# Performance work log

Hardware: AMD Instinct MI355X
Metric: run time of the kernel (lower is better)

## Reference

```python
import jax, jax.numpy as jnp
import numpy as np

S, B, E, H = 2048, 4, 512, 8
HD = E // H


def setup_inputs() -> dict:
    key = jax.random.key(0)
    ks = jax.random.split(key, 5)
    scale = 1.0 / np.sqrt(E)
    return {
        "query": jax.random.normal(ks[0], (S, B, E), jnp.float32),
        "key": jax.random.normal(ks[1], (S, B, E), jnp.float32),
        "value": jax.random.normal(ks[2], (S, B, E), jnp.float32),
        "in_proj_weight": jax.random.normal(ks[3], (3 * E, E), jnp.float32) * scale,
        "in_proj_bias": jnp.zeros((3 * E,), jnp.float32),
        "out_proj_weight": jax.random.normal(ks[4], (E, E), jnp.float32) * scale,
        "out_proj_bias": jnp.zeros((E,), jnp.float32),
    }


def reference(query, key, value, in_proj_weight, in_proj_bias, out_proj_weight, out_proj_bias):
    tgt_len, bsz, embed_dim = query.shape
    src_len = key.shape[0]
    # Quirk of this module: first chunk (w_qk) projects BOTH q and k; third chunk projects v.
    w_qk = in_proj_weight[:embed_dim]
    w_v = in_proj_weight[2 * embed_dim:]
    b_qk = in_proj_bias[:embed_dim]
    b_v = in_proj_bias[2 * embed_dim:]
    q = query @ w_qk.T + b_qk          # [S, B, E]
    k = key @ w_qk.T + b_qk
    v = value @ w_v.T + b_v
    # (S, B, E) -> (B*H, S, HD)
    def split_heads(x, n):
        return x.reshape(n, bsz * H, HD).transpose(1, 0, 2)
    q = split_heads(q, tgt_len) / jnp.sqrt(jnp.asarray(HD, q.dtype))
    k = split_heads(k, src_len)
    v = split_heads(v, src_len)
    scores = jnp.einsum("bqd,bkd->bqk", q, k)          # [B*H, S, S] full score matrix
    attn = jax.nn.softmax(scores, axis=-1)
    out = jnp.einsum("bqk,bkd->bqd", attn, v)          # [B*H, S, HD]
    out = out.transpose(1, 0, 2).reshape(tgt_len * bsz, embed_dim)
    out = out @ out_proj_weight.T + out_proj_bias
    return out.reshape(tgt_len, bsz, embed_dim)
```

## Files before the change

### kernel.cpp

```cpp
#include <hip/hip_runtime.h>
#include <hip/hip_bf16.h>

typedef __attribute__((ext_vector_type(8))) short s16x8;
typedef __attribute__((ext_vector_type(4))) short s16x4;
typedef __attribute__((ext_vector_type(4))) float f32x4;

#if __has_builtin(__builtin_amdgcn_exp2f)
#define EXP2F(x) __builtin_amdgcn_exp2f(x)
#else
#define EXP2F(x) exp2f(x)
#endif

#define S_LEN 2048
#define EMB   512
#define MROWS 8192

__device__ __forceinline__ short f2bf(float f) {
    union { float f; unsigned u; } z; z.f = f;
    unsigned r = z.u + 0x7FFF + ((z.u >> 16) & 1);
    return (short)(r >> 16);
}
__device__ __forceinline__ short f2bf_fast(float f) {
    union { float f; unsigned u; } z; z.f = f;
    return (short)((z.u + 0x8000u) >> 16);
}
__device__ __forceinline__ int swzs(int s) { return s ^ ((s >> 3) & 7); }

template<int AF32, int BF32>
__device__ __forceinline__ void gemm_mainloop(const void* __restrict__ Ag,
                                              const void* __restrict__ Bg,
                                              short* sA, short* sB,
                                              f32x4 acc[2][4], int K)
{
    const int tid  = threadIdx.x;
    const int lane = tid & 63;
    const int wv   = tid >> 6;
    const int lsw  = lane ^ ((lane >> 3) & 7);
    const int amt  = (wv >> 1) * 2;
    const int bnt  = (wv & 1) * 4;

    const int brow = tid >> 2, bqd = tid & 3;
    const int boff = swzs((brow >> 4) * 64 + bqd * 16 + (brow & 15)) * 8;
    const int frow = tid >> 3, ffc = tid & 7;
    const int foff = swzs((frow >> 4) * 64 + (ffc >> 1) * 16 + (frow & 15)) * 8
                   + (ffc & 1) * 4;

    f32x4 afr[2], bfr[2];
    s16x8 ahr, bhr;

    auto loadT = [&](const void* G, int kt, f32x4* fr, s16x8& hr, int F32) {
        if (F32) {
            const float* g = (const float*)G + (size_t)frow * K + kt + ffc * 4;
            fr[0] = *(const f32x4*)g;
            fr[1] = *(const f32x4*)(g + (size_t)64 * K);
        } else {
            hr = *(const s16x8*)((const short*)G + (size_t)brow * K + kt + bqd * 8);
        }
    };
    auto commitT = [&](short* s, f32x4* fr, s16x8& hr, int F32) {
        if (F32) {
#pragma unroll
            for (int p = 0; p < 2; ++p) {
                s16x4 o4;
                o4[0] = f2bf_fast(fr[p][0]); o4[1] = f2bf_fast(fr[p][1]);
                o4[2] = f2bf_fast(fr[p][2]); o4[3] = f2bf_fast(fr[p][3]);
                *(s16x4*)(s + foff + p * 2048) = o4;
            }
        } else {
            *(s16x8*)(s + boff) = hr;
        }
    };

    loadT(Ag, 0, afr, ahr, AF32);
    loadT(Bg, 0, bfr, bhr, BF32);
    commitT(sA, afr, ahr, AF32);
    commitT(sB, bfr, bhr, BF32);
    __syncthreads();

    int cur = 0;
    for (int kt = 0; kt < K; kt += 32) {
        const int ktn = (kt + 32 < K) ? kt + 32 : 0;
        loadT(Ag, ktn, afr, ahr, AF32);
        loadT(Bg, ktn, bfr, bhr, BF32);

        const short* sAc = sA + cur * 4096;
        const short* sBc = sB + cur * 4096;
        s16x8 aF[2], bF[4];
#pragma unroll
        for (int i = 0; i < 2; ++i)
            aF[i] = *(const s16x8*)(sAc + ((amt + i) * 64 + lsw) * 8);
#pragma unroll
        for (int j = 0; j < 4; ++j)
            bF[j] = *(const s16x8*)(sBc + ((bnt + j) * 64 + lsw) * 8);
#pragma unroll
        for (int i = 0; i < 2; ++i)
#pragma unroll
            for (int j = 0; j < 4; ++j)
                acc[i][j] = __builtin_amdgcn_mfma_f32_16x16x32_bf16(aF[i], bF[j], acc[i][j], 0, 0, 0);

        commitT(sA + (cur ^ 1) * 4096, afr, ahr, AF32);
        commitT(sB + (cur ^ 1) * 4096, bfr, bhr, BF32);
        __syncthreads();
        cur ^= 1;
    }
}

__global__ __launch_bounds__(512, 4) void qkv_proj(const float* __restrict__ query,
                                                   const float* __restrict__ key,
                                                   const float* __restrict__ value,
                                                   const float* __restrict__ W,
                                                   const float* __restrict__ bias,
                                                   short* __restrict__ q,
                                                   short* __restrict__ k,
                                                   short* __restrict__ vt)
{
    __shared__ __align__(16) short smem[16384];
    short* sA = smem;
    short* sB = smem + 8192;

    const int z = blockIdx.z;
    const float* X  = (z == 0) ? query : (z == 1) ? key : value;
    const float* Wz = W    + (z == 2 ? (size_t)1024 * EMB : 0);
    const float* bz = bias + (z == 2 ? 1024 : 0);
    const float scale = (z == 0) ? 0.125f * 1.44269504f : 1.0f;

    const int blockM = blockIdx.x * 128, blockN = blockIdx.y * 128;

    f32x4 acc[2][4];
#pragma unroll
    for (int i = 0; i < 2; ++i)
#pragma unroll
        for (int j = 0; j < 4; ++j)
            acc[i][j] = (f32x4){0.f, 0.f, 0.f, 0.f};

    gemm_mainloop<1, 1>(X + (size_t)blockM * EMB, Wz + (size_t)blockN * EMB,
                        sA, sB, acc, EMB);

    const int tid = threadIdx.x, lane = tid & 63, wv = tid >> 6;
    const int l15 = lane & 15, quad = lane >> 4;
    const int wm = (wv >> 1) * 32, wn = (wv & 1) * 64;

#pragma unroll
    for (int j = 0; j < 4; ++j) {
        int colL = wn + j * 16 + l15;
        float bval = bz[blockN + colL];
        int hL = colL >> 6, hd = colL & 63;
#pragma unroll
        for (int i = 0; i < 2; ++i) {
#pragma unroll
            for (int r = 0; r < 4; ++r) {
                int rowL = wm + i * 16 + quad * 4 + r;
                int b = rowL & 3, sp = rowL >> 2;
                float val = (acc[i][j][r] + bval) * scale;
                int idx;
                if (z == 2) {
                    int R = (b * 2 + hL) * 64 + hd;
                    idx = R * 32 + (((sp >> 3) ^ (R & 3)) << 3) + (sp & 7);
                } else {
                    idx = ((b * 2 + hL) * 32 + sp) * 64 + hd;
                }
                smem[idx] = f2bf(val);
            }
        }
    }
    __syncthreads();

    if (z == 2) {
        int R = tid;
        int b = tid >> 7, hL = (tid >> 6) & 1, hd = tid & 63;
        int h = (blockN >> 6) + hL;
        short* dst = vt + ((size_t)(b * 8 + h) * 64 + hd) * 2048 + (blockM >> 2);
#pragma unroll
        for (int u = 0; u < 4; ++u)
            ((s16x8*)dst)[u] = *(const s16x8*)(smem + R * 32 + ((u ^ (R & 3)) << 3));
    } else {
        const s16x8* src = (const s16x8*)(smem + tid * 32);
        int b = tid >> 7, hL = (tid >> 6) & 1;
        int sp = (tid >> 1) & 31, hdh = (tid & 1) * 32;
        int h = (blockN >> 6) + hL;
        short* dstp = (z == 0) ? q : k;
        short* dst = dstp + ((size_t)(b * 8 + h) * 2048 + (blockM >> 2) + sp) * 64 + hdh;
#pragma unroll
        for (int u = 0; u < 4; ++u) ((s16x8*)dst)[u] = src[u];
    }
}

__global__ __launch_bounds__(256, 2) void flash_attn(const short* __restrict__ q,
                                                     const short* __restrict__ k,
                                                     const short* __restrict__ vt,
                                                     short* __restrict__ attn)
{
    __shared__ __align__(16) short sK[2][4096];
    __shared__ __align__(16) short sV[2][4096];
    const int bh = blockIdx.x;
    const int q0 = blockIdx.y * 128;
    const int tid = threadIdx.x, wv = tid >> 6, lane = tid & 63;
    const int l15 = lane & 15, quad = lane >> 4;
    const int lsw = lane ^ ((lane >> 3) & 7);

    s16x8 qf[2][2];
#pragma unroll
    for (int qr = 0; qr < 2; ++qr) {
        const short* qp = q + ((size_t)(bh * 2048 + q0 + wv * 32 + qr * 16 + l15)) * 64 + quad * 8;
        qf[qr][0] = *(const s16x8*)qp;
        qf[qr][1] = *(const s16x8*)(qp + 32);
    }

    const short* kg = k  + (size_t)bh * 2048 * 64;
    const short* vg = vt + (size_t)bh * 64 * 2048;

    const int rk = tid >> 2, qd = tid & 3;
    const int pr = (rk & 35) | ((rk & 24) >> 1) | ((rk & 4) << 2);
    const int kw0 = swzs((pr >> 4) * 64 + qd * 16 + (pr & 15)) * 8;
    const int vw0 = swzs((rk >> 4) * 64 + qd * 16 + (rk & 15)) * 8;
    const short* kgt = kg + (size_t)rk * 64 + qd * 8;
    const short* vgt = vg + (size_t)rk * 2048 + qd * 8;

    f32x4 o[2][4];
    float ls[2][4];
#pragma unroll
    for (int qr = 0; qr < 2; ++qr)
#pragma unroll
        for (int i = 0; i < 4; ++i) { o[qr][i] = (f32x4){0.f, 0.f, 0.f, 0.f}; ls[qr][i] = 0.f; }

    s16x8 ka = *(const s16x8*)(kgt);
    s16x8 kb = *(const s16x8*)(kgt + 32);
    s16x8 va = *(const s16x8*)(vgt);
    s16x8 vb = *(const s16x8*)(vgt + 32);
    *(s16x8*)(sK[0] + kw0)        = ka;
    *(s16x8*)(sK[0] + kw0 + 2048) = kb;
    *(s16x8*)(sV[0] + vw0)        = va;
    *(s16x8*)(sV[0] + vw0 + 2048) = vb;
    __syncthreads();

    int cur = 0;
    for (int kt = 0; kt < 2048; kt += 64) {
        const int ktn = (kt + 64) & 2047;
        ka = *(const s16x8*)(kgt + (size_t)ktn * 64);
        kb = *(const s16x8*)(kgt + (size_t)ktn * 64 + 32);
        va = *(const s16x8*)(vgt + ktn);
        vb = *(const s16x8*)(vgt + ktn + 32);

        const short* Kc = sK[cur];
        const short* Vc = sV[cur];

        f32x4 sc[2][4];
#pragma unroll
        for (int ct = 0; ct < 4; ++ct) {
            s16x8 kf0 = *(const s16x8*)(Kc + (ct * 64 + lsw) * 8);
            s16x8 kf1 = *(const s16x8*)(Kc + (ct * 64 + lsw) * 8 + 2048);
#pragma unroll
            for (int qr = 0; qr < 2; ++qr) {
                f32x4 c = (f32x4){0.f, 0.f, 0.f, 0.f};
                c = __builtin_amdgcn_mfma_f32_16x16x32_bf16(kf0, qf[qr][0], c, 0, 0, 0);
                c = __builtin_amdgcn_mfma_f32_16x16x32_bf16(kf1, qf[qr][1], c, 0, 0, 0);
                sc[qr][ct] = c;
            }
        }
        s16x8 pf[2][2];
#pragma unroll
        for (int qr = 0; qr < 2; ++qr)
#pragma unroll
            for (int c = 0; c < 2; ++c)
#pragma unroll
                for (int h = 0; h < 2; ++h)
#pragma unroll
                    for (int r = 0; r < 4; ++r) {
                        float p = EXP2F(sc[qr][2 * c + h][r]);
                        ls[qr][r] += p;
                        pf[qr][c][h * 4 + r] = f2bf_fast(p);
                    }
#pragma unroll
        for (int nt = 0; nt < 4; ++nt)
#pragma unroll
            for (int c = 0; c < 2; ++c) {
                s16x8 vf = *(const s16x8*)(Vc + ((c * 4 + nt) * 64 + lsw) * 8);
#pragma unroll
                for (int qr = 0; qr < 2; ++qr)
                    o[qr][nt] = __builtin_amdgcn_mfma_f32_16x16x32_bf16(pf[qr][c], vf, o[qr][nt], 0, 0, 0);
            }
        *(s16x8*)(sK[cur ^ 1] + kw0)        = ka;
        *(s16x8*)(sK[cur ^ 1] + kw0 + 2048) = kb;
        *(s16x8*)(sV[cur ^ 1] + vw0)        = va;
        *(s16x8*)(sV[cur ^ 1] + vw0 + 2048) = vb;
        __syncthreads();
        cur ^= 1;
    }

    const int b = bh >> 3, h = bh & 7;
#pragma unroll
    for (int qr = 0; qr < 2; ++qr) {
        float s = ls[qr][0] + ls[qr][1] + ls[qr][2] + ls[qr][3];
        s += __shfl_xor(s, 16, 64);
        s += __shfl_xor(s, 32, 64);
        float sinv = 1.0f / s;
        float inv[4];
#pragma unroll
        for (int r = 0; r < 4; ++r)
            inv[r] = __shfl(sinv, quad * 20 + r, 64);
#pragma unroll
        for (int r = 0; r < 4; ++r) {
            int srow = q0 + wv * 32 + qr * 16 + quad * 4 + r;
#pragma unroll
            for (int nt = 0; nt < 4; ++nt)
                attn[(size_t)(srow * 4 + b) * 512 + h * 64 + nt * 16 + l15] = f2bf(o[qr][nt][r] * inv[r]);
        }
    }
}

__global__ __launch_bounds__(512, 4) void out_proj(const short* __restrict__ attn,
                                                   const float* __restrict__ W,
                                                   const float* __restrict__ bias,
                                                   float* __restrict__ out)
{
    __shared__ __align__(16) short sA[2 * 4096], sB[2 * 4096];
    const int blockM = blockIdx.x * 128, blockN = blockIdx.y * 128;

    f32x4 acc[2][4];
#pragma unroll
    for (int i = 0; i < 2; ++i)
#pragma unroll
        for (int j = 0; j < 4; ++j)
            acc[i][j] = (f32x4){0.f, 0.f, 0.f, 0.f};

    gemm_mainloop<0, 1>(attn + (size_t)blockM * EMB, W + (size_t)blockN * EMB,
                        sA, sB, acc, EMB);

    const int tid = threadIdx.x, lane = tid & 63, wv = tid >> 6;
    const int l15 = lane & 15, quad = lane >> 4;
    const int wm = (wv >> 1) * 32, wn = (wv & 1) * 64;

#pragma unroll
    for (int j = 0; j < 4; ++j) {
        int col = blockN + wn + j * 16 + l15;
        float bval = bias[col];
#pragma unroll
        for (int i = 0; i < 2; ++i) {
#pragma unroll
            for (int r = 0; r < 4; ++r) {
                int row = blockM + wm + i * 16 + quad * 4 + r;
                out[(size_t)row * 512 + col] = acc[i][j][r] + bval;
            }
        }
    }
}

extern "C" void kernel_launch(void* const* d_in, const int* in_sizes, int n_in,
                              void* d_out, int out_size, void* d_ws, size_t ws_size,
                              hipStream_t stream)
{
    const float* query = (const float*)d_in[0];
    const float* key   = (const float*)d_in[1];
    const float* value = (const float*)d_in[2];
    const float* ipw   = (const float*)d_in[3];
    const float* ipb   = (const float*)d_in[4];
    const float* opw   = (const float*)d_in[5];
    const float* opb   = (const float*)d_in[6];
    float* out = (float*)d_out;

    const size_t NELEM = (size_t)MROWS * EMB;
    short* q    = (short*)d_ws;
    short* k    = q + NELEM;
    short* attn = k + NELEM;
    short* vt   = (short*)d_out;

    qkv_proj  <<<dim3(64, 4, 3), 512, 0, stream>>>(query, key, value, ipw, ipb, q, k, vt);
    flash_attn<<<dim3(32, 16),   256, 0, stream>>>(q, k, vt, attn);
    out_proj  <<<dim3(64, 4),    512, 0, stream>>>(attn, opw, opb, out);
}
```

Baseline: 202.9 us.

## Pre-convert projection weights to bf16 and deepen GEMM prefetch to two stages

```diff
diff --git a/kernel.cpp b/kernel.cpp
--- a/kernel.cpp
+++ b/kernel.cpp
@@ -25,6 +25,20 @@
     return (short)((z.u + 0x8000u) >> 16);
 }
 __device__ __forceinline__ int swzs(int s) { return s ^ ((s >> 3) & 7); }
+
+__global__ __launch_bounds__(256) void w_to_bf16(const float* __restrict__ W,
+                                                 short* __restrict__ wb, int n)
+{
+    int i = (blockIdx.x * 256 + threadIdx.x) * 8;
+    if (i < n) {
+        f32x4 a = *(const f32x4*)(W + i);
+        f32x4 b = *(const f32x4*)(W + i + 4);
+        s16x8 o;
+        o[0] = f2bf(a[0]); o[1] = f2bf(a[1]); o[2] = f2bf(a[2]); o[3] = f2bf(a[3]);
+        o[4] = f2bf(b[0]); o[5] = f2bf(b[1]); o[6] = f2bf(b[2]); o[7] = f2bf(b[3]);
+        *(s16x8*)(wb + i) = o;
+    }
+}
 
 template<int AF32, int BF32>
 __device__ __forceinline__ void gemm_mainloop(const void* __restrict__ Ag,
@@ -45,19 +59,28 @@
     const int foff = swzs((frow >> 4) * 64 + (ffc >> 1) * 16 + (frow & 15)) * 8
                    + (ffc & 1) * 4;
 
-    f32x4 afr[2], bfr[2];
-    s16x8 ahr, bhr;
-
-    auto loadT = [&](const void* G, int kt, f32x4* fr, s16x8& hr, int F32) {
-        if (F32) {
-            const float* g = (const float*)G + (size_t)frow * K + kt + ffc * 4;
+    f32x4 aF0[2], aF1[2], bF0[2], bF1[2];
+    s16x8 aH0, aH1, bH0, bH1;
+
+    auto loadA = [&](int kt, f32x4 fr[2], s16x8& hr) {
+        if (AF32) {
+            const float* g = (const float*)Ag + (size_t)frow * K + kt + ffc * 4;
             fr[0] = *(const f32x4*)g;
             fr[1] = *(const f32x4*)(g + (size_t)64 * K);
         } else {
-            hr = *(const s16x8*)((const short*)G + (size_t)brow * K + kt + bqd * 8);
+            hr = *(const s16x8*)((const short*)Ag + (size_t)brow * K + kt + bqd * 8);
         }
     };
-    auto commitT = [&](short* s, f32x4* fr, s16x8& hr, int F32) {
+    auto loadB = [&](int kt, f32x4 fr[2], s16x8& hr) {
+        if (BF32) {
+            const float* g = (const float*)Bg + (size_t)frow * K + kt + ffc * 4;
+            fr[0] = *(const f32x4*)g;
+            fr[1] = *(const f32x4*)(g + (size_t)64 * K);
+        } else {
+            hr = *(const s16x8*)((const short*)Bg + (size_t)brow * K + kt + bqd * 8);
+        }
+    };
+    auto commit = [&](short* s, f32x4 fr[2], s16x8& hr, int F32) {
         if (F32) {
 #pragma unroll
             for (int p = 0; p < 2; ++p) {
@@ -70,45 +93,44 @@
             *(s16x8*)(s + boff) = hr;
         }
     };
-
-    loadT(Ag, 0, afr, ahr, AF32);
-    loadT(Bg, 0, bfr, bhr, BF32);
-    commitT(sA, afr, ahr, AF32);
-    commitT(sB, bfr, bhr, BF32);
+    auto compute = [&](const short* sAc, const short* sBc) {
+        s16x8 a[2], b[4];
+#pragma unroll
+        for (int i = 0; i < 2; ++i)
+            a[i] = *(const s16x8*)(sAc + ((amt + i) * 64 + lsw) * 8);
+#pragma unroll
+        for (int j = 0; j < 4; ++j)
+            b[j] = *(const s16x8*)(sBc + ((bnt + j) * 64 + lsw) * 8);
+#pragma unroll
+        for (int i = 0; i < 2; ++i)
+#pragma unroll
+            for (int j = 0; j < 4; ++j)
+                acc[i][j] = __builtin_amdgcn_mfma_f32_16x16x32_bf16(a[i], b[j], acc[i][j], 0, 0, 0);
+    };
+
+    loadA(0, aF0, aH0);  loadB(0, bF0, bH0);
+    loadA(32, aF1, aH1); loadB(32, bF1, bH1);
+    commit(sA, aF0, aH0, AF32); commit(sB, bF0, bH0, BF32);
     __syncthreads();
 
-    int cur = 0;
-    for (int kt = 0; kt < K; kt += 32) {
-        const int ktn = (kt + 32 < K) ? kt + 32 : 0;
-        loadT(Ag, ktn, afr, ahr, AF32);
-        loadT(Bg, ktn, bfr, bhr, BF32);
-
-        const short* sAc = sA + cur * 4096;
-        const short* sBc = sB + cur * 4096;
-        s16x8 aF[2], bF[4];
-#pragma unroll
-        for (int i = 0; i < 2; ++i)
-            aF[i] = *(const s16x8*)(sAc + ((amt + i) * 64 + lsw) * 8);
-#pragma unroll
-        for (int j = 0; j < 4; ++j)
-            bF[j] = *(const s16x8*)(sBc + ((bnt + j) * 64 + lsw) * 8);
-#pragma unroll
-        for (int i = 0; i < 2; ++i)
-#pragma unroll
-            for (int j = 0; j < 4; ++j)
-                acc[i][j] = __builtin_amdgcn_mfma_f32_16x16x32_bf16(aF[i], bF[j], acc[i][j], 0, 0, 0);
-
-        commitT(sA + (cur ^ 1) * 4096, afr, ahr, AF32);
-        commitT(sB + (cur ^ 1) * 4096, bfr, bhr, BF32);
+    for (int kt = 0; kt < K; kt += 64) {
+        const int k2 = (kt + 64 < K) ? kt + 64 : 0;
+        loadA(k2, aF0, aH0); loadB(k2, bF0, bH0);
+        compute(sA, sB);
+        commit(sA + 4096, aF1, aH1, AF32); commit(sB + 4096, bF1, bH1, BF32);
         __syncthreads();
-        cur ^= 1;
+        const int k3 = (kt + 96 < K) ? kt + 96 : 0;
+        loadA(k3, aF1, aH1); loadB(k3, bF1, bH1);
+        compute(sA + 4096, sB + 4096);
+        commit(sA, aF0, aH0, AF32); commit(sB, bF0, bH0, BF32);
+        __syncthreads();
     }
 }
 
 __global__ __launch_bounds__(512, 4) void qkv_proj(const float* __restrict__ query,
                                                    const float* __restrict__ key,
                                                    const float* __restrict__ value,
-                                                   const float* __restrict__ W,
+                                                   const short* __restrict__ wb,
                                                    const float* __restrict__ bias,
                                                    short* __restrict__ q,
                                                    short* __restrict__ k,
@@ -120,7 +142,7 @@
 
     const int z = blockIdx.z;
     const float* X  = (z == 0) ? query : (z == 1) ? key : value;
-    const float* Wz = W    + (z == 2 ? (size_t)1024 * EMB : 0);
+    const short* Wz = wb   + (z == 2 ? (size_t)1024 * EMB : 0);
     const float* bz = bias + (z == 2 ? 1024 : 0);
     const float scale = (z == 0) ? 0.125f * 1.44269504f : 1.0f;
 
@@ -133,7 +155,7 @@
         for (int j = 0; j < 4; ++j)
             acc[i][j] = (f32x4){0.f, 0.f, 0.f, 0.f};
 
-    gemm_mainloop<1, 1>(X + (size_t)blockM * EMB, Wz + (size_t)blockN * EMB,
+    gemm_mainloop<1, 0>(X + (size_t)blockM * EMB, Wz + (size_t)blockN * EMB,
                         sA, sB, acc, EMB);
 
     const int tid = threadIdx.x, lane = tid & 63, wv = tid >> 6;
@@ -363,8 +385,10 @@
     short* k    = q + NELEM;
     short* attn = k + NELEM;
     short* vt   = (short*)d_out;
-
-    qkv_proj  <<<dim3(64, 4, 3), 512, 0, stream>>>(query, key, value, ipw, ipb, q, k, vt);
+    short* wb   = (short*)d_out + NELEM;
+
+    w_to_bf16 <<<dim3(384),      256, 0, stream>>>(ipw, wb, 1536 * EMB);
+    qkv_proj  <<<dim3(64, 4, 3), 512, 0, stream>>>(query, key, value, wb, ipb, q, k, vt);
     flash_attn<<<dim3(32, 16),   256, 0, stream>>>(q, k, vt, attn);
     out_proj  <<<dim3(64, 4),    512, 0, stream>>>(attn, opw, opb, out);
 }
```

Result: faster. 187.0 us (-7.8%).
